# Performance work log

Measured on AMD Instinct MI355X. Metric: run time of the kernel, lower is better.

Reference implementation:

```python
import jax, jax.numpy as jnp
import numpy as np

EPS = 1e-12
H = 128  # lstm_hidden_unit_num


def _ln(z, g, b):
    mu = jnp.mean(z, axis=-1, keepdims=True)
    var = jnp.mean((z - mu) ** 2, axis=-1, keepdims=True)
    return (z - mu) * jax.lax.rsqrt(var + EPS) * g + b


def _lstm(x, W, lng, lnb):
    # LayerNormBasicLSTMCell(activation=relu, forget_bias=1, no matmul bias).
    # x: [B,T,D]; W: [D+H, 4H]; lng/lnb: [5,H] (i, j, f, o, cell-state LN)
    B = x.shape[0]

    def step(carry, xt):
        c, h = carry
        z = jnp.concatenate([xt, h], axis=-1) @ W  # [B, 4H]
        i, j, f, o = jnp.split(z, 4, axis=-1)
        i = _ln(i, lng[0], lnb[0])
        j = _ln(j, lng[1], lnb[1])
        f = _ln(f, lng[2], lnb[2])
        o = _ln(o, lng[3], lnb[3])
        new_c = c * jax.nn.sigmoid(f + 1.0) + jax.nn.sigmoid(i) * jax.nn.relu(j)
        new_h = jax.nn.relu(_ln(new_c, lng[4], lnb[4])) * jax.nn.sigmoid(o)
        return (new_c, new_h), new_h

    init = (jnp.zeros((B, H), x.dtype), jnp.zeros((B, H), x.dtype))
    _, hs = jax.lax.scan(step, init, jnp.swapaxes(x, 0, 1))
    return jnp.swapaxes(hs, 0, 1)  # [B,T,H]


def _attn(out, v, Wo, bo):
    # softmax attention over time, then dense(512, relu)
    alpha = jax.nn.softmax(jnp.einsum('bth,h->bt', out, v), axis=-1)
    ctx = jnp.einsum('bt,bth->bh', alpha, out)
    return jax.nn.relu(ctx @ Wo + bo)


def setup_inputs() -> dict:
    key = jax.random.key(0)
    ks = jax.random.split(key, 12)
    B, T, V, E = 128, 46, 8150, 300
    norm_gain = 0.8
    d = {}
    d['x1'] = jax.random.normal(ks[0], (B, T, V), jnp.float32)
    d['x2'] = jax.random.normal(ks[1], (B, T, V), jnp.float32)
    d['embed1'] = jax.random.normal(ks[2], (V, E), jnp.float32) * 0.05
    d['embed2'] = jax.random.normal(ks[3], (V, E), jnp.float32) * 0.05
    d['W_lstm1'] = jax.random.normal(ks[4], (E + H, 4 * H), jnp.float32) * 0.05
    d['W_lstm2'] = jax.random.normal(ks[5], (E + H, 4 * H), jnp.float32) * 0.05
    d['lng1'] = jnp.full((5, H), norm_gain, jnp.float32)
    d['lnb1'] = jnp.zeros((5, H), jnp.float32)
    d['lng2'] = jnp.full((5, H), norm_gain, jnp.float32)
    d['lnb2'] = jnp.zeros((5, H), jnp.float32)
    d['attn_v1'] = jax.random.normal(ks[6], (H,), jnp.float32)
    d['attn_Wo1'] = jax.random.normal(ks[7], (H, 512), jnp.float32) * 0.05
    d['attn_bo1'] = jnp.zeros((512,), jnp.float32)
    d['attn_v2'] = jax.random.normal(ks[8], (H,), jnp.float32)
    d['attn_Wo2'] = jax.random.normal(ks[9], (H, 512), jnp.float32) * 0.05
    d['attn_bo2'] = jnp.zeros((512,), jnp.float32)
    d['W_h'] = jax.random.normal(ks[10], (1024, 512), jnp.float32) * 0.05
    d['b_h'] = jnp.zeros((512,), jnp.float32)
    d['W_out'] = jax.random.normal(ks[11], (512, 2), jnp.float32) * 0.05
    d['b_out'] = jnp.zeros((2,), jnp.float32)
    return d


def reference(x1, x2, embed1, embed2, W_lstm1, W_lstm2, lng1, lnb1, lng2, lnb2,
              attn_v1, attn_Wo1, attn_bo1, attn_v2, attn_Wo2, attn_bo2,
              W_h, b_h, W_out, b_out):
    e1 = jnp.einsum('btv,ve->bte', x1, embed1)  # [B,46,300]
    e2 = jnp.einsum('btv,ve->bte', x2, embed2)
    o1 = _lstm(e1, W_lstm1, lng1, lnb1)         # [B,46,128]
    o2 = _lstm(e2, W_lstm2, lng2, lnb2)
    a1 = _attn(o1, attn_v1, attn_Wo1, attn_bo1)  # [B,512]
    a2 = _attn(o2, attn_v2, attn_Wo2, attn_bo2)
    hidden = jax.nn.relu(jnp.concatenate([a1, a2], axis=1) @ W_h + b_h)
    logits = hidden @ W_out + b_out              # [B,2]
    return logits
```

## Files before the change

### kernel.cpp

```cpp
#include <hip/hip_runtime.h>
#include <math.h>

typedef short bf16x8 __attribute__((ext_vector_type(8)));
typedef float f32x4 __attribute__((ext_vector_type(4)));

__device__ __forceinline__ ushort f2bf(float f) {
    unsigned u = __float_as_uint(f);
    u = u + 0x7FFFu + ((u >> 16) & 1u);
    return (ushort)(u >> 16);
}
__device__ __forceinline__ float bf2f(ushort h) {
    return __uint_as_float(((unsigned)h) << 16);
}

#define LSTRIDE 40

__global__ __launch_bounds__(256) void trans_kernel(
    const float* __restrict__ embed, ushort* __restrict__ Et_hi,
    ushort* __restrict__ Et_lo) {
    __shared__ float tile[64][65];
    int k0 = blockIdx.x * 64;
    int n0 = blockIdx.y * 64;
    int tid = threadIdx.x;
#pragma unroll
    for (int i = 0; i < 16; i++) {
        int idx = tid + i * 256;
        int r = idx >> 6, c = idx & 63;
        int gk = k0 + r, gn = n0 + c;
        float v = (gk < 8150 && gn < 300) ? embed[(size_t)gk * 300 + gn] : 0.f;
        tile[r][c] = v;
    }
    __syncthreads();
#pragma unroll
    for (int i = 0; i < 16; i++) {
        int idx = tid + i * 256;
        int n = idx >> 6, k = idx & 63;
        float v = tile[k][n];
        ushort h = f2bf(v);
        Et_hi[(size_t)(n0 + n) * 8192 + k0 + k] = h;
        Et_lo[(size_t)(n0 + n) * 8192 + k0 + k] = f2bf(v - bf2f(h));
    }
}

__global__ __launch_bounds__(512, 4) void e_kernel(
    const float* __restrict__ X, const ushort* __restrict__ Et_hi,
    const ushort* __restrict__ Et_lo, float* __restrict__ Eo) {
    __shared__ ushort Ah[128 * LSTRIDE], Al[128 * LSTRIDE];
    __shared__ ushort Bh[160 * LSTRIDE], Bl[160 * LSTRIDE];
    int bm = blockIdx.x * 128;
    int bn = blockIdx.y * 160;
    int kc = blockIdx.z * 1024;
    int tid = threadIdx.x;
    int lane = tid & 63, w = tid >> 6;
    int quad = lane >> 4, l16 = lane & 15;
    int wm = (w & 3) * 32, wn = (w >> 2) * 80;

    f32x4 acc[2][5];
#pragma unroll
    for (int a = 0; a < 2; a++)
#pragma unroll
        for (int b = 0; b < 5; b++) acc[a][b] = (f32x4){0.f, 0.f, 0.f, 0.f};

    for (int step = 0; step < 32; step++) {
        int k0 = kc + step * 32;
#pragma unroll
        for (int r = 0; r < 4; r++) {
            int flat = tid + r * 512;
            int m = flat >> 4, kk = (flat & 15) * 2;
            int gk = k0 + kk;
            float vx = 0.f, vy = 0.f;
            if (gk + 1 < 8150) {
                float2 v = *(const float2*)&X[(size_t)(bm + m) * 8150 + gk];
                vx = v.x; vy = v.y;
            }
            ushort hx = f2bf(vx), hy = f2bf(vy);
            ushort2 h; h.x = hx; h.y = hy;
            ushort2 l; l.x = f2bf(vx - bf2f(hx)); l.y = f2bf(vy - bf2f(hy));
            *(ushort2*)&Ah[m * LSTRIDE + kk] = h;
            *(ushort2*)&Al[m * LSTRIDE + kk] = l;
        }
#pragma unroll
        for (int r = 0; r < 2; r++) {
            int flat = tid + r * 512;
            if (flat < 640) {
                int n = flat >> 2, seg = flat & 3;
                size_t go = (size_t)(bn + n) * 8192 + k0 + seg * 8;
                *(uint4*)&Bh[n * LSTRIDE + seg * 8] = *(const uint4*)&Et_hi[go];
                *(uint4*)&Bl[n * LSTRIDE + seg * 8] = *(const uint4*)&Et_lo[go];
            }
        }
        __syncthreads();
        bf16x8 a_h[2], a_l[2];
#pragma unroll
        for (int mf = 0; mf < 2; mf++) {
            int row = wm + mf * 16 + l16;
            a_h[mf] = *(const bf16x8*)&Ah[row * LSTRIDE + quad * 8];
            a_l[mf] = *(const bf16x8*)&Al[row * LSTRIDE + quad * 8];
        }
#pragma unroll
        for (int nf = 0; nf < 5; nf++) {
            int col = wn + nf * 16 + l16;
            bf16x8 b_h = *(const bf16x8*)&Bh[col * LSTRIDE + quad * 8];
            bf16x8 b_l = *(const bf16x8*)&Bl[col * LSTRIDE + quad * 8];
#pragma unroll
            for (int mf = 0; mf < 2; mf++) {
                acc[mf][nf] = __builtin_amdgcn_mfma_f32_16x16x32_bf16(a_h[mf], b_h, acc[mf][nf], 0, 0, 0);
                acc[mf][nf] = __builtin_amdgcn_mfma_f32_16x16x32_bf16(a_h[mf], b_l, acc[mf][nf], 0, 0, 0);
                acc[mf][nf] = __builtin_amdgcn_mfma_f32_16x16x32_bf16(a_l[mf], b_h, acc[mf][nf], 0, 0, 0);
            }
        }
        __syncthreads();
    }
#pragma unroll
    for (int mf = 0; mf < 2; mf++)
#pragma unroll
        for (int nf = 0; nf < 5; nf++) {
            int row = bm + wm + mf * 16 + quad * 4;
            int col = bn + wn + nf * 16 + l16;
#pragma unroll
            for (int i = 0; i < 4; i++)
                atomicAdd(&Eo[(size_t)(row + i) * 320 + col], acc[mf][nf][i]);
        }
}

__global__ __launch_bounds__(512, 4) void ze_kernel(
    const float* __restrict__ Eo, const float* __restrict__ W,
    float* __restrict__ Zx) {
    __shared__ ushort Ah[128 * LSTRIDE], Al[128 * LSTRIDE];
    __shared__ ushort Bh[128 * LSTRIDE], Bl[128 * LSTRIDE];
    int bm = blockIdx.x * 128;
    int bn = blockIdx.y * 128;
    int tid = threadIdx.x;
    int lane = tid & 63, w = tid >> 6;
    int quad = lane >> 4, l16 = lane & 15;
    int wm = (w & 3) * 32, wn = (w >> 2) * 64;

    f32x4 acc[2][4];
#pragma unroll
    for (int a = 0; a < 2; a++)
#pragma unroll
        for (int b = 0; b < 4; b++) acc[a][b] = (f32x4){0.f, 0.f, 0.f, 0.f};

    for (int k0 = 0; k0 < 320; k0 += 32) {
#pragma unroll
        for (int r = 0; r < 2; r++) {
            int flat = tid + r * 512;
            int m = flat >> 3, kk4 = (flat & 7) * 4;
            float4 v = *(const float4*)&Eo[(size_t)(bm + m) * 320 + k0 + kk4];
            ushort4 h, l;
            h.x = f2bf(v.x); l.x = f2bf(v.x - bf2f(h.x));
            h.y = f2bf(v.y); l.y = f2bf(v.y - bf2f(h.y));
            h.z = f2bf(v.z); l.z = f2bf(v.z - bf2f(h.z));
            h.w = f2bf(v.w); l.w = f2bf(v.w - bf2f(h.w));
            *(ushort4*)&Ah[m * LSTRIDE + kk4] = h;
            *(ushort4*)&Al[m * LSTRIDE + kk4] = l;
        }
#pragma unroll
        for (int p = 0; p < 8; p++) {
            int kk = (tid >> 7) + p * 4;
            int n = tid & 127;
            int gk = k0 + kk;
            float v = (gk < 300) ? W[(size_t)gk * 512 + bn + n] : 0.f;
            ushort h = f2bf(v);
            Bh[n * LSTRIDE + kk] = h;
            Bl[n * LSTRIDE + kk] = f2bf(v - bf2f(h));
        }
        __syncthreads();
        bf16x8 a_h[2], a_l[2];
#pragma unroll
        for (int mf = 0; mf < 2; mf++) {
            int row = wm + mf * 16 + l16;
            a_h[mf] = *(const bf16x8*)&Ah[row * LSTRIDE + quad * 8];
            a_l[mf] = *(const bf16x8*)&Al[row * LSTRIDE + quad * 8];
        }
#pragma unroll
        for (int nf = 0; nf < 4; nf++) {
            int col = wn + nf * 16 + l16;
            bf16x8 b_h = *(const bf16x8*)&Bh[col * LSTRIDE + quad * 8];
            bf16x8 b_l = *(const bf16x8*)&Bl[col * LSTRIDE + quad * 8];
#pragma unroll
            for (int mf = 0; mf < 2; mf++) {
                acc[mf][nf] = __builtin_amdgcn_mfma_f32_16x16x32_bf16(a_h[mf], b_h, acc[mf][nf], 0, 0, 0);
                acc[mf][nf] = __builtin_amdgcn_mfma_f32_16x16x32_bf16(a_h[mf], b_l, acc[mf][nf], 0, 0, 0);
                acc[mf][nf] = __builtin_amdgcn_mfma_f32_16x16x32_bf16(a_l[mf], b_h, acc[mf][nf], 0, 0, 0);
            }
        }
        __syncthreads();
    }
#pragma unroll
    for (int mf = 0; mf < 2; mf++)
#pragma unroll
        for (int nf = 0; nf < 4; nf++) {
            int row = bm + wm + mf * 16 + quad * 4;
            int col = bn + wn + nf * 16 + l16;
#pragma unroll
            for (int i = 0; i < 4; i++)
                Zx[(size_t)(row + i) * 512 + col] = acc[mf][nf][i];
        }
}

#define TT 46

__device__ __forceinline__ float sigf(float x) { return 1.f / (1.f + expf(-x)); }

__global__ __launch_bounds__(256) void lstm_kernel(
    const float* __restrict__ Zx1, const float* __restrict__ Zx2,
    const float* __restrict__ W1, const float* __restrict__ W2,
    const float* __restrict__ lng1, const float* __restrict__ lnb1,
    const float* __restrict__ lng2, const float* __restrict__ lnb2,
    float* __restrict__ o1, float* __restrict__ o2) {
    int lstm = blockIdx.x >> 5;
    int r0 = (blockIdx.x & 31) * 4;
    const float* Zx = lstm ? Zx2 : Zx1;
    const float* Wh = (lstm ? W2 : W1) + 300 * 512;
    const float* g  = lstm ? lng2 : lng1;
    const float* bb = lstm ? lnb2 : lnb1;
    float* obuf = lstm ? o2 : o1;

    __shared__ __align__(16) float hs[4][128];
    __shared__ __align__(16) float cs[4][128];
    __shared__ __align__(16) float zb[4][512];
    __shared__ float mu[4][4], rs[4][4], cmu[4], crs[4];

    int tid = threadIdx.x;
    for (int i = tid; i < 512; i += 256) {
        hs[i >> 7][i & 127] = 0.f;
        cs[i >> 7][i & 127] = 0.f;
    }
    __syncthreads();

    for (int t = 0; t < TT; t++) {
        int c0 = tid * 2;
        float2 acc[4];
#pragma unroll
        for (int r = 0; r < 4; r++)
            acc[r] = *(const float2*)&Zx[((size_t)(r0 + r) * TT + t) * 512 + c0];
        for (int k = 0; k < 128; k += 4) {
            float4 h4[4];
#pragma unroll
            for (int r = 0; r < 4; r++) h4[r] = *(const float4*)&hs[r][k];
#pragma unroll
            for (int kk = 0; kk < 4; kk++) {
                float2 wv = *(const float2*)&Wh[(size_t)(k + kk) * 512 + c0];
#pragma unroll
                for (int r = 0; r < 4; r++) {
                    float hk = ((const float*)&h4[r])[kk];
                    acc[r].x = fmaf(hk, wv.x, acc[r].x);
                    acc[r].y = fmaf(hk, wv.y, acc[r].y);
                }
            }
        }
#pragma unroll
        for (int r = 0; r < 4; r++) {
            zb[r][c0] = acc[r].x;
            zb[r][c0 + 1] = acc[r].y;
        }
        __syncthreads();

        {
            int grp = tid >> 4;
            int row = grp >> 2, gate = grp & 3;
            int l = tid & 15;
            float s = 0.f, ss = 0.f;
#pragma unroll
            for (int j = 0; j < 8; j++) {
                float v = zb[row][gate * 128 + l + j * 16];
                s += v; ss += v * v;
            }
#pragma unroll
            for (int off = 1; off < 16; off <<= 1) {
                s += __shfl_xor(s, off);
                ss += __shfl_xor(ss, off);
            }
            if (l == 0) {
                float m_ = s * (1.f / 128.f);
                mu[row][gate] = m_;
                rs[row][gate] = rsqrtf(ss * (1.f / 128.f) - m_ * m_ + 1e-12f);
            }
        }
        __syncthreads();

        float ogate[2];
#pragma unroll
        for (int ii = 0; ii < 2; ii++) {
            int idx = tid + ii * 256;
            int row = idx >> 7, col = idx & 127;
            float i_g = (zb[row][col]       - mu[row][0]) * rs[row][0] * g[0 * 128 + col] + bb[0 * 128 + col];
            float j_g = (zb[row][128 + col] - mu[row][1]) * rs[row][1] * g[1 * 128 + col] + bb[1 * 128 + col];
            float f_g = (zb[row][256 + col] - mu[row][2]) * rs[row][2] * g[2 * 128 + col] + bb[2 * 128 + col];
            float o_g = (zb[row][384 + col] - mu[row][3]) * rs[row][3] * g[3 * 128 + col] + bb[3 * 128 + col];
            float nc = cs[row][col] * sigf(f_g + 1.f) + sigf(i_g) * fmaxf(j_g, 0.f);
            cs[row][col] = nc;
            ogate[ii] = o_g;
        }
        __syncthreads();

        {
            int ww = tid >> 6, l = tid & 63;
            float v0 = cs[ww][l], v1 = cs[ww][l + 64];
            float s = v0 + v1, ss = v0 * v0 + v1 * v1;
#pragma unroll
            for (int off = 1; off < 64; off <<= 1) {
                s += __shfl_xor(s, off);
                ss += __shfl_xor(ss, off);
            }
            if (l == 0) {
                float m_ = s * (1.f / 128.f);
                cmu[ww] = m_;
                crs[ww] = rsqrtf(ss * (1.f / 128.f) - m_ * m_ + 1e-12f);
            }
        }
        __syncthreads();

#pragma unroll
        for (int ii = 0; ii < 2; ii++) {
            int idx = tid + ii * 256;
            int row = idx >> 7, col = idx & 127;
            float lnc = (cs[row][col] - cmu[row]) * crs[row] * g[4 * 128 + col] + bb[4 * 128 + col];
            float hv = fmaxf(lnc, 0.f) * sigf(ogate[ii]);
            hs[row][col] = hv;
            obuf[((size_t)(r0 + row) * TT + t) * 128 + col] = hv;
        }
        __syncthreads();
    }
}

__global__ __launch_bounds__(256) void attn_kernel(
    const float* __restrict__ o1, const float* __restrict__ o2,
    const float* __restrict__ v1, const float* __restrict__ v2,
    const float* __restrict__ Wo1, const float* __restrict__ Wo2,
    const float* __restrict__ bo1, const float* __restrict__ bo2,
    float* __restrict__ acat) {
    int lstm = blockIdx.x >> 7;
    int b = blockIdx.x & 127;
    const float* o  = (lstm ? o2 : o1) + (size_t)b * TT * 128;
    const float* v  = lstm ? v2 : v1;
    const float* Wo = lstm ? Wo2 : Wo1;
    const float* bo = lstm ? bo2 : bo1;
    __shared__ float sc[64];
    __shared__ float ctx[128];
    int tid = threadIdx.x;
    if (tid < TT) {
        float s = 0.f;
        for (int h = 0; h < 128; h++) s = fmaf(o[tid * 128 + h], v[h], s);
        sc[tid] = s;
    }
    __syncthreads();
    if (tid < 64) {
        float x = (tid < TT) ? sc[tid] : -1e30f;
        float m = x;
#pragma unroll
        for (int off = 1; off < 64; off <<= 1) m = fmaxf(m, __shfl_xor(m, off));
        float e = (tid < TT) ? expf(x - m) : 0.f;
        float s = e;
#pragma unroll
        for (int off = 1; off < 64; off <<= 1) s += __shfl_xor(s, off);
        if (tid < TT) sc[tid] = e / s;
    }
    __syncthreads();
    if (tid < 128) {
        float s = 0.f;
        for (int t = 0; t < TT; t++) s = fmaf(sc[t], o[t * 128 + tid], s);
        ctx[tid] = s;
    }
    __syncthreads();
#pragma unroll
    for (int j = 0; j < 2; j++) {
        int n = tid * 2 + j;
        float s = bo[n];
        for (int h = 0; h < 128; h++) s = fmaf(ctx[h], Wo[h * 512 + n], s);
        acat[(size_t)b * 1024 + lstm * 512 + n] = fmaxf(s, 0.f);
    }
}

__global__ __launch_bounds__(256) void final_kernel(
    const float* __restrict__ acat, const float* __restrict__ Wh,
    const float* __restrict__ bh, const float* __restrict__ Wout,
    const float* __restrict__ bout, float* __restrict__ out) {
    int b = blockIdx.x;
    __shared__ float ain[1024];
    __shared__ float hid[512];
    __shared__ float red[4];
    int tid = threadIdx.x;
    for (int i = tid; i < 1024; i += 256) ain[i] = acat[(size_t)b * 1024 + i];
    __syncthreads();
#pragma unroll
    for (int j = 0; j < 2; j++) {
        int n = tid * 2 + j;
        float s = bh[n];
        for (int k = 0; k < 1024; k++) s = fmaf(ain[k], Wh[(size_t)k * 512 + n], s);
        hid[n] = fmaxf(s, 0.f);
    }
    __syncthreads();
    for (int j = 0; j < 2; j++) {
        float p = 0.f;
        for (int k = tid; k < 512; k += 256) p = fmaf(hid[k], Wout[k * 2 + j], p);
#pragma unroll
        for (int off = 1; off < 64; off <<= 1) p += __shfl_xor(p, off);
        if ((tid & 63) == 0) red[tid >> 6] = p;
        __syncthreads();
        if (tid == 0) out[b * 2 + j] = red[0] + red[1] + red[2] + red[3] + bout[j];
        __syncthreads();
    }
}

extern "C" void kernel_launch(void* const* d_in, const int* in_sizes, int n_in,
                              void* d_out, int out_size, void* d_ws, size_t ws_size,
                              hipStream_t stream) {
    const float* x1      = (const float*)d_in[0];
    const float* x2      = (const float*)d_in[1];
    const float* embed1  = (const float*)d_in[2];
    const float* embed2  = (const float*)d_in[3];
    const float* W_lstm1 = (const float*)d_in[4];
    const float* W_lstm2 = (const float*)d_in[5];
    const float* lng1    = (const float*)d_in[6];
    const float* lnb1    = (const float*)d_in[7];
    const float* lng2    = (const float*)d_in[8];
    const float* lnb2    = (const float*)d_in[9];
    const float* attn_v1 = (const float*)d_in[10];
    const float* attn_Wo1= (const float*)d_in[11];
    const float* attn_bo1= (const float*)d_in[12];
    const float* attn_v2 = (const float*)d_in[13];
    const float* attn_Wo2= (const float*)d_in[14];
    const float* attn_bo2= (const float*)d_in[15];
    const float* W_h     = (const float*)d_in[16];
    const float* b_h     = (const float*)d_in[17];
    const float* W_out   = (const float*)d_in[18];
    const float* b_out   = (const float*)d_in[19];
    float* out = (float*)d_out;

    ushort* Et_hi = (ushort*)d_ws;
    ushort* Et_lo = Et_hi + (size_t)320 * 8192;
    float* Eo  = (float*)(Et_lo + (size_t)320 * 8192);
    float* Zx1 = Eo + (size_t)5888 * 320;
    float* Zx2 = Zx1 + 3014656;
    float* o1  = Zx2 + 3014656;
    float* o2  = o1 + 753664;
    float* acat = o2 + 753664;

    hipMemsetAsync(Eo, 0, (size_t)5888 * 320 * 4, stream);
    trans_kernel<<<dim3(128, 5), 256, 0, stream>>>(embed1, Et_hi, Et_lo);
    e_kernel<<<dim3(46, 2, 8), 512, 0, stream>>>(x1, Et_hi, Et_lo, Eo);
    ze_kernel<<<dim3(46, 4), 512, 0, stream>>>(Eo, W_lstm1, Zx1);
    hipMemsetAsync(Eo, 0, (size_t)5888 * 320 * 4, stream);
    trans_kernel<<<dim3(128, 5), 256, 0, stream>>>(embed2, Et_hi, Et_lo);
    e_kernel<<<dim3(46, 2, 8), 512, 0, stream>>>(x2, Et_hi, Et_lo, Eo);
    ze_kernel<<<dim3(46, 4), 512, 0, stream>>>(Eo, W_lstm2, Zx2);

    lstm_kernel<<<64, 256, 0, stream>>>(Zx1, Zx2, W_lstm1, W_lstm2,
                                        lng1, lnb1, lng2, lnb2, o1, o2);
    attn_kernel<<<256, 256, 0, stream>>>(o1, o2, attn_v1, attn_v2,
                                         attn_Wo1, attn_Wo2, attn_bo1, attn_bo2, acat);
    final_kernel<<<128, 256, 0, stream>>>(acat, W_h, b_h, W_out, b_out, out);
}
```

Before: 1.297 ms.

## Register-prefetch next K tile in embedding GEMM and double split-K

The embedding GEMM kernel now loads the next K-step's X and embedding tiles into registers while MFMAs run on the current shared-memory tile, then writes them to LDS after a barrier. This is meant to hide global-memory latency that was previously exposed before each compute phase. The split-K factor also doubles from 8 to 16 chunks of 512, giving more blocks for occupancy. In exchange, each output element gets twice as many atomicAdds, and the kernel uses more registers and an extra barrier per step.

```diff
diff --git a/kernel.cpp b/kernel.cpp
--- a/kernel.cpp
+++ b/kernel.cpp
@@ -49,7 +49,7 @@
     __shared__ ushort Bh[160 * LSTRIDE], Bl[160 * LSTRIDE];
     int bm = blockIdx.x * 128;
     int bn = blockIdx.y * 160;
-    int kc = blockIdx.z * 1024;
+    int kc = blockIdx.z * 512;
     int tid = threadIdx.x;
     int lane = tid & 63, w = tid >> 6;
     int quad = lane >> 4, l16 = lane & 15;
@@ -61,18 +61,38 @@
 #pragma unroll
         for (int b = 0; b < 5; b++) acc[a][b] = (f32x4){0.f, 0.f, 0.f, 0.f};
 
-    for (int step = 0; step < 32; step++) {
-        int k0 = kc + step * 32;
+    float2 aReg[4];
+    uint4 bRegH[2], bRegL[2];
+
+    auto loadA = [&](int k0) {
 #pragma unroll
         for (int r = 0; r < 4; r++) {
             int flat = tid + r * 512;
             int m = flat >> 4, kk = (flat & 15) * 2;
             int gk = k0 + kk;
-            float vx = 0.f, vy = 0.f;
-            if (gk + 1 < 8150) {
-                float2 v = *(const float2*)&X[(size_t)(bm + m) * 8150 + gk];
-                vx = v.x; vy = v.y;
-            }
+            float2 v = make_float2(0.f, 0.f);
+            if (gk + 1 < 8150) v = *(const float2*)&X[(size_t)(bm + m) * 8150 + gk];
+            aReg[r] = v;
+        }
+    };
+    auto loadB = [&](int k0) {
+#pragma unroll
+        for (int r = 0; r < 2; r++) {
+            int flat = tid + r * 512;
+            if (flat < 640) {
+                int n = flat >> 2, seg = flat & 3;
+                size_t go = (size_t)(bn + n) * 8192 + k0 + seg * 8;
+                bRegH[r] = *(const uint4*)&Et_hi[go];
+                bRegL[r] = *(const uint4*)&Et_lo[go];
+            }
+        }
+    };
+    auto writeAB = [&]() {
+#pragma unroll
+        for (int r = 0; r < 4; r++) {
+            int flat = tid + r * 512;
+            int m = flat >> 4, kk = (flat & 15) * 2;
+            float vx = aReg[r].x, vy = aReg[r].y;
             ushort hx = f2bf(vx), hy = f2bf(vy);
             ushort2 h; h.x = hx; h.y = hy;
             ushort2 l; l.x = f2bf(vx - bf2f(hx)); l.y = f2bf(vy - bf2f(hy));
@@ -84,12 +104,24 @@
             int flat = tid + r * 512;
             if (flat < 640) {
                 int n = flat >> 2, seg = flat & 3;
-                size_t go = (size_t)(bn + n) * 8192 + k0 + seg * 8;
-                *(uint4*)&Bh[n * LSTRIDE + seg * 8] = *(const uint4*)&Et_hi[go];
-                *(uint4*)&Bl[n * LSTRIDE + seg * 8] = *(const uint4*)&Et_lo[go];
-            }
-        }
-        __syncthreads();
+                *(uint4*)&Bh[n * LSTRIDE + seg * 8] = bRegH[r];
+                *(uint4*)&Bl[n * LSTRIDE + seg * 8] = bRegL[r];
+            }
+        }
+    };
+
+    loadA(kc);
+    loadB(kc);
+    writeAB();
+    asm volatile("s_waitcnt lgkmcnt(0)" ::: "memory");
+    __builtin_amdgcn_s_barrier();
+
+    for (int step = 0; step < 16; step++) {
+        if (step < 15) {
+            int k0n = kc + (step + 1) * 32;
+            loadA(k0n);
+            loadB(k0n);
+        }
         bf16x8 a_h[2], a_l[2];
 #pragma unroll
         for (int mf = 0; mf < 2; mf++) {
@@ -109,8 +141,15 @@
                 acc[mf][nf] = __builtin_amdgcn_mfma_f32_16x16x32_bf16(a_l[mf], b_h, acc[mf][nf], 0, 0, 0);
             }
         }
-        __syncthreads();
-    }
+        asm volatile("s_waitcnt lgkmcnt(0)" ::: "memory");
+        __builtin_amdgcn_s_barrier();
+        if (step < 15) {
+            writeAB();
+            asm volatile("s_waitcnt lgkmcnt(0)" ::: "memory");
+        }
+        __builtin_amdgcn_s_barrier();
+    }
+
 #pragma unroll
     for (int mf = 0; mf < 2; mf++)
 #pragma unroll
@@ -440,11 +479,11 @@
 
     hipMemsetAsync(Eo, 0, (size_t)5888 * 320 * 4, stream);
     trans_kernel<<<dim3(128, 5), 256, 0, stream>>>(embed1, Et_hi, Et_lo);
-    e_kernel<<<dim3(46, 2, 8), 512, 0, stream>>>(x1, Et_hi, Et_lo, Eo);
+    e_kernel<<<dim3(46, 2, 16), 512, 0, stream>>>(x1, Et_hi, Et_lo, Eo);
     ze_kernel<<<dim3(46, 4), 512, 0, stream>>>(Eo, W_lstm1, Zx1);
     hipMemsetAsync(Eo, 0, (size_t)5888 * 320 * 4, stream);
     trans_kernel<<<dim3(128, 5), 256, 0, stream>>>(embed2, Et_hi, Et_lo);
-    e_kernel<<<dim3(46, 2, 8), 512, 0, stream>>>(x2, Et_hi, Et_lo, Eo);
+    e_kernel<<<dim3(46, 2, 16), 512, 0, stream>>>(x2, Et_hi, Et_lo, Eo);
     ze_kernel<<<dim3(46, 4), 512, 0, stream>>>(Eo, W_lstm2, Zx2);
 
     lstm_kernel<<<64, 256, 0, stream>>>(Zx1, Zx2, W_lstm1, W_lstm2,
```

Result: slower. 1.402 ms (+8.1%).

## Register-prefetch next K tile in embedding GEMM and double split-K depth

Applied to the files above, without the earlier changes.

The embedding GEMM kernel now loads the next 32-wide K slice of X and the split embedding table into registers while the MFMAs for the current slice run, then converts and writes them to LDS after a barrier. It also raises MFMA issue priority around the compute loop and halves the per-block K range, launching twice as many split-K blocks. The aim is to hide global load latency and fill the GPU better with more blocks. The cost is more registers per thread and twice as many atomicAdd reductions into the output.

```diff
diff --git a/kernel.cpp b/kernel.cpp
--- a/kernel.cpp
+++ b/kernel.cpp
@@ -49,47 +49,83 @@
     __shared__ ushort Bh[160 * LSTRIDE], Bl[160 * LSTRIDE];
     int bm = blockIdx.x * 128;
     int bn = blockIdx.y * 160;
-    int kc = blockIdx.z * 1024;
+    int kc = blockIdx.z * 512;
     int tid = threadIdx.x;
     int lane = tid & 63, w = tid >> 6;
     int quad = lane >> 4, l16 = lane & 15;
     int wm = (w & 3) * 32, wn = (w >> 2) * 80;
 
+    int mA0 = tid >> 4, kA0 = (tid & 15) * 2;
+    const float* xb0 = X + (size_t)(bm + mA0) * 8150 + kA0;
+    const float* xb1 = xb0 + (size_t)32 * 8150;
+    const float* xb2 = xb1 + (size_t)32 * 8150;
+    const float* xb3 = xb2 + (size_t)32 * 8150;
+    int lA0 = mA0 * LSTRIDE + kA0;
+    int nB0 = tid >> 2, segB = tid & 3;
+    size_t ebOff = (size_t)(bn + nB0) * 8192 + segB * 8;
+    const ushort* ebh0 = Et_hi + ebOff;
+    const ushort* ebl0 = Et_lo + ebOff;
+    int lB0 = nB0 * LSTRIDE + segB * 8;
+    const bool bsec = (tid < 128);
+    const bool guard = (kc + 512 > 8150);
+
     f32x4 acc[2][5];
 #pragma unroll
     for (int a = 0; a < 2; a++)
 #pragma unroll
         for (int b = 0; b < 5; b++) acc[a][b] = (f32x4){0.f, 0.f, 0.f, 0.f};
 
-    for (int step = 0; step < 32; step++) {
-        int k0 = kc + step * 32;
-#pragma unroll
-        for (int r = 0; r < 4; r++) {
-            int flat = tid + r * 512;
-            int m = flat >> 4, kk = (flat & 15) * 2;
-            int gk = k0 + kk;
-            float vx = 0.f, vy = 0.f;
-            if (gk + 1 < 8150) {
-                float2 v = *(const float2*)&X[(size_t)(bm + m) * 8150 + gk];
-                vx = v.x; vy = v.y;
-            }
-            ushort hx = f2bf(vx), hy = f2bf(vy);
-            ushort2 h; h.x = hx; h.y = hy;
-            ushort2 l; l.x = f2bf(vx - bf2f(hx)); l.y = f2bf(vy - bf2f(hy));
-            *(ushort2*)&Ah[m * LSTRIDE + kk] = h;
-            *(ushort2*)&Al[m * LSTRIDE + kk] = l;
-        }
-#pragma unroll
-        for (int r = 0; r < 2; r++) {
-            int flat = tid + r * 512;
-            if (flat < 640) {
-                int n = flat >> 2, seg = flat & 3;
-                size_t go = (size_t)(bn + n) * 8192 + k0 + seg * 8;
-                *(uint4*)&Bh[n * LSTRIDE + seg * 8] = *(const uint4*)&Et_hi[go];
-                *(uint4*)&Bl[n * LSTRIDE + seg * 8] = *(const uint4*)&Et_lo[go];
-            }
-        }
-        __syncthreads();
+    float2 a0, a1, a2, a3;
+    uint4 bh0, bh1, bl0, bl1;
+
+#define LOADAB(k0)                                                            \
+    do {                                                                      \
+        if (!guard || ((k0) + kA0 + 1 < 8150)) {                              \
+            a0 = *(const float2*)(xb0 + (k0));                                \
+            a1 = *(const float2*)(xb1 + (k0));                                \
+            a2 = *(const float2*)(xb2 + (k0));                                \
+            a3 = *(const float2*)(xb3 + (k0));                                \
+        } else {                                                              \
+            a0 = make_float2(0.f, 0.f); a1 = a0; a2 = a0; a3 = a0;            \
+        }                                                                     \
+        bh0 = *(const uint4*)(ebh0 + (k0));                                   \
+        bl0 = *(const uint4*)(ebl0 + (k0));                                   \
+        if (bsec) {                                                           \
+            bh1 = *(const uint4*)(ebh0 + (size_t)128 * 8192 + (k0));          \
+            bl1 = *(const uint4*)(ebl0 + (size_t)128 * 8192 + (k0));          \
+        }                                                                     \
+    } while (0)
+
+#define CVT1(v, H, L)                                                         \
+    do { ushort hx = f2bf((v).x), hy = f2bf((v).y);                           \
+         (H).x = hx; (H).y = hy;                                              \
+         (L).x = f2bf((v).x - bf2f(hx)); (L).y = f2bf((v).y - bf2f(hy)); } while (0)
+
+#define WRITEAB()                                                             \
+    do {                                                                      \
+        ushort2 h0, l0, h1, l1, h2, l2, h3, l3;                               \
+        CVT1(a0, h0, l0); CVT1(a1, h1, l1); CVT1(a2, h2, l2); CVT1(a3, h3, l3);\
+        *(ushort2*)&Ah[lA0] = h0;                 *(ushort2*)&Al[lA0] = l0;   \
+        *(ushort2*)&Ah[lA0 + 32 * LSTRIDE] = h1;  *(ushort2*)&Al[lA0 + 32 * LSTRIDE] = l1; \
+        *(ushort2*)&Ah[lA0 + 64 * LSTRIDE] = h2;  *(ushort2*)&Al[lA0 + 64 * LSTRIDE] = l2; \
+        *(ushort2*)&Ah[lA0 + 96 * LSTRIDE] = h3;  *(ushort2*)&Al[lA0 + 96 * LSTRIDE] = l3; \
+        *(uint4*)&Bh[lB0] = bh0; *(uint4*)&Bl[lB0] = bl0;                     \
+        if (bsec) {                                                           \
+            *(uint4*)&Bh[lB0 + 128 * LSTRIDE] = bh1;                          \
+            *(uint4*)&Bl[lB0 + 128 * LSTRIDE] = bl1;                          \
+        }                                                                     \
+    } while (0)
+
+    LOADAB(kc);
+    WRITEAB();
+    asm volatile("s_waitcnt lgkmcnt(0)" ::: "memory");
+    __builtin_amdgcn_s_barrier();
+
+    for (int step = 0; step < 16; step++) {
+        if (step < 15) {
+            int k0n = kc + (step + 1) * 32;
+            LOADAB(k0n);
+        }
         bf16x8 a_h[2], a_l[2];
 #pragma unroll
         for (int mf = 0; mf < 2; mf++) {
@@ -97,6 +133,7 @@
             a_h[mf] = *(const bf16x8*)&Ah[row * LSTRIDE + quad * 8];
             a_l[mf] = *(const bf16x8*)&Al[row * LSTRIDE + quad * 8];
         }
+        __builtin_amdgcn_s_setprio(1);
 #pragma unroll
         for (int nf = 0; nf < 5; nf++) {
             int col = wn + nf * 16 + l16;
@@ -109,8 +146,19 @@
                 acc[mf][nf] = __builtin_amdgcn_mfma_f32_16x16x32_bf16(a_l[mf], b_h, acc[mf][nf], 0, 0, 0);
             }
         }
-        __syncthreads();
-    }
+        __builtin_amdgcn_s_setprio(0);
+        asm volatile("s_waitcnt lgkmcnt(0)" ::: "memory");
+        __builtin_amdgcn_s_barrier();
+        if (step < 15) {
+            WRITEAB();
+            asm volatile("s_waitcnt lgkmcnt(0)" ::: "memory");
+        }
+        __builtin_amdgcn_s_barrier();
+    }
+#undef LOADAB
+#undef CVT1
+#undef WRITEAB
+
 #pragma unroll
     for (int mf = 0; mf < 2; mf++)
 #pragma unroll
@@ -440,11 +488,11 @@
 
     hipMemsetAsync(Eo, 0, (size_t)5888 * 320 * 4, stream);
     trans_kernel<<<dim3(128, 5), 256, 0, stream>>>(embed1, Et_hi, Et_lo);
-    e_kernel<<<dim3(46, 2, 8), 512, 0, stream>>>(x1, Et_hi, Et_lo, Eo);
+    e_kernel<<<dim3(46, 2, 16), 512, 0, stream>>>(x1, Et_hi, Et_lo, Eo);
     ze_kernel<<<dim3(46, 4), 512, 0, stream>>>(Eo, W_lstm1, Zx1);
     hipMemsetAsync(Eo, 0, (size_t)5888 * 320 * 4, stream);
     trans_kernel<<<dim3(128, 5), 256, 0, stream>>>(embed2, Et_hi, Et_lo);
-    e_kernel<<<dim3(46, 2, 8), 512, 0, stream>>>(x2, Et_hi, Et_lo, Eo);
+    e_kernel<<<dim3(46, 2, 16), 512, 0, stream>>>(x2, Et_hi, Et_lo, Eo);
     ze_kernel<<<dim3(46, 4), 512, 0, stream>>>(Eo, W_lstm2, Zx2);
 
     lstm_kernel<<<64, 256, 0, stream>>>(Zx1, Zx2, W_lstm1, W_lstm2,
```

Result: faster. 1.132 ms (-12.8%).
